# Kernel optimization log

Measured on AMD Instinct MI355X. Metric: run time of the kernel, lower is better.

The kernel has to match this reference:

```python
import jax, jax.numpy as jnp
import numpy as np

B, N, FEA = 4, 200000, 9
G = 32                      # per-axis index range used for voxel keys
NUM_SEG = B * G * G * G     # 131072 = max possible unique voxels (static)
OUT_DIM, COMPRE = 256, 16
BN_EPS = 1e-5

def _glorot(k, shape):
    lim = float(np.sqrt(6.0 / (shape[0] + shape[1])))
    return jax.random.uniform(k, shape, jnp.float32, -lim, lim)

def setup_inputs() -> dict:
    key = jax.random.key(0)
    ks = jax.random.split(key, 16)
    inp = {
        "pt_fea": jax.random.normal(ks[0], (B, N, FEA), jnp.float32),
        "xy_ind": jax.random.randint(ks[1], (B, N, 3), 0, G, dtype=jnp.int32),
    }
    dims = [FEA, 64, 128, 256, OUT_DIM]
    bn_dims = [FEA, 64, 128, 256]
    for i, d in enumerate(bn_dims):
        inp[f"bn{i}_g"] = jnp.ones((d,), jnp.float32)
        inp[f"bn{i}_b"] = jnp.zeros((d,), jnp.float32)
        inp[f"bn{i}_m"] = jax.random.normal(ks[2 + i], (d,), jnp.float32) * 0.1
        inp[f"bn{i}_v"] = jnp.ones((d,), jnp.float32)
    for i in range(4):
        inp[f"w{i+1}"] = _glorot(ks[6 + i], (dims[i], dims[i + 1]))
        inp[f"b{i+1}"] = jnp.zeros((dims[i + 1],), jnp.float32)
    inp["wc"] = _glorot(ks[10], (OUT_DIM, COMPRE))
    inp["bc"] = jnp.zeros((COMPRE,), jnp.float32)
    return inp

def _bn(x, g, b, m, v):
    return (x - m) * jax.lax.rsqrt(v + BN_EPS) * g + b

def reference(pt_fea, xy_ind, bn0_g, bn0_b, bn0_m, bn0_v,
              bn1_g, bn1_b, bn1_m, bn1_v, bn2_g, bn2_b, bn2_m, bn2_v,
              bn3_g, bn3_b, bn3_m, bn3_v,
              w1, b1, w2, b2, w3, b3, w4, b4, wc, bc):
    # flatten batched point clouds; build scalar voxel key = (batch, ix, iy, iz)
    b_idx = jnp.broadcast_to(jnp.arange(B, dtype=jnp.int32)[:, None], (B, N)).reshape(-1)
    ind = xy_ind.reshape(B * N, 3)
    keys = ((b_idx * G + ind[:, 0]) * G + ind[:, 1]) * G + ind[:, 2]  # [B*N]
    fea = pt_fea.reshape(B * N, FEA)

    # torch.unique(dim=0) equivalent: sorted unique keys + inverse map (static size)
    unq_keys, unq_inv = jnp.unique(keys, size=NUM_SEG, fill_value=-1, return_inverse=True)

    # torch_scatter.scatter_max over voxels
    pooled = jax.ops.segment_max(fea, unq_inv, num_segments=NUM_SEG)
    cnt = jax.ops.segment_sum(jnp.ones((B * N,), jnp.float32), unq_inv, num_segments=NUM_SEG)
    pooled = jnp.where(cnt[:, None] > 0, pooled, 0.0)  # neutralize empty padding slots (-inf)

    # PPmodel: BN -> Linear -> BN -> ReLU (x3) -> Linear (eval-mode BatchNorm)
    x = _bn(pooled, bn0_g, bn0_b, bn0_m, bn0_v)
    x = jax.nn.relu(_bn(x @ w1 + b1, bn1_g, bn1_b, bn1_m, bn1_v))
    x = jax.nn.relu(_bn(x @ w2 + b2, bn2_g, bn2_b, bn2_m, bn2_v))
    x = jax.nn.relu(_bn(x @ w3 + b3, bn3_g, bn3_b, bn3_m, bn3_v))
    x = x @ w4 + b4
    out = jax.nn.relu(x @ wc + bc)  # fea_compression

    # decode keys back to [num_vox, 4] int64 (batch, ix, iy, iz); padding rows = -1
    valid = unq_keys >= 0
    kk = jnp.where(valid, unq_keys, 0)
    unq = jnp.stack([kk // (G * G * G), (kk // (G * G)) % G, (kk // G) % G, kk % G], axis=1)
    unq = jnp.where(valid[:, None], unq, -1)
    return unq.astype(jnp.int64), out
```

## Files before the change

### kernel.cpp

```cpp
#include <hip/hip_runtime.h>

#define NPTS   800000
#define NPB    200000
#define NSEG   131072
#define OUT_OFF (NSEG*4)
#define BN_EPS 1e-5f
#define BCAP   3072

typedef __attribute__((ext_vector_type(8))) __bf16 bf16x8;
typedef __attribute__((ext_vector_type(4))) float  f32x4;

#define MFMA16 __builtin_amdgcn_mfma_f32_16x16x32_bf16

__device__ __forceinline__ unsigned short f2bf(float f) {
    unsigned u = __float_as_uint(f);
    u += 0x7fffu + ((u >> 16) & 1u);
    return (unsigned short)(u >> 16);
}
__device__ __forceinline__ unsigned encf(float f) {
    unsigned u = __float_as_uint(f);
    return (u & 0x80000000u) ? ~u : (u | 0x80000000u);
}
__device__ __forceinline__ float decf(unsigned e) {
    unsigned u = (e & 0x80000000u) ? (e & 0x7FFFFFFFu) : ~e;
    return __uint_as_float(u);
}

__global__ void k_fold(const float* __restrict__ g0, const float* __restrict__ be0,
                       const float* __restrict__ m0, const float* __restrict__ v0,
                       const float* __restrict__ g1, const float* __restrict__ be1,
                       const float* __restrict__ m1, const float* __restrict__ v1,
                       const float* __restrict__ g2, const float* __restrict__ be2,
                       const float* __restrict__ m2, const float* __restrict__ v2,
                       const float* __restrict__ g3, const float* __restrict__ be3,
                       const float* __restrict__ m3, const float* __restrict__ v3,
                       const float* __restrict__ w1, const float* __restrict__ b1,
                       const float* __restrict__ w2, const float* __restrict__ b2,
                       const float* __restrict__ w3, const float* __restrict__ b3,
                       const float* __restrict__ w4, const float* __restrict__ b4,
                       const float* __restrict__ wc, const float* __restrict__ bc,
                       unsigned short* __restrict__ WT1, float* __restrict__ c1,
                       unsigned short* __restrict__ WT2, float* __restrict__ c2,
                       unsigned short* __restrict__ WT3, float* __restrict__ c3,
                       unsigned short* __restrict__ WT4, float* __restrict__ c4,
                       unsigned* __restrict__ bucketFill) {
    int id = blockIdx.x * 256 + threadIdx.x;
    if (id < 32768) {
        int j = id >> 7, k = id & 127;
        float s = g3[j] * rsqrtf(v3[j] + BN_EPS);
        WT3[id] = f2bf(w3[k*256 + j] * s);
    } else if (id < 40960) {
        int t = id - 32768; int j = t >> 6, k = t & 63;
        float s = g2[j] * rsqrtf(v2[j] + BN_EPS);
        WT2[t] = f2bf(w2[k*128 + j] * s);
    } else if (id < 45056) {
        int t = id - 40960; int j = t >> 8, k = t & 255;
        float acc = 0.f;
        for (int i = 0; i < 256; ++i) acc += w4[k*256 + i] * wc[i*16 + j];
        WT4[t] = f2bf(acc);
    } else if (id < 47104) {
        int t = id - 45056; int j = t >> 5, k = t & 31;
        float val = 0.f;
        if (k < 9) {
            float s0 = g0[k] * rsqrtf(v0[k] + BN_EPS);
            float s1 = g1[j] * rsqrtf(v1[j] + BN_EPS);
            val = s0 * w1[k*64 + j] * s1;
        }
        WT1[t] = f2bf(val);
    } else if (id < 47168) {
        int j = id - 47104;
        float s1 = g1[j] * rsqrtf(v1[j] + BN_EPS);
        float acc = b1[j];
        for (int k = 0; k < 9; ++k) {
            float s0 = g0[k] * rsqrtf(v0[k] + BN_EPS);
            float t0 = be0[k] - m0[k] * s0;
            acc += t0 * w1[k*64 + j];
        }
        c1[j] = (acc - m1[j]) * s1 + be1[j];
    } else if (id < 47296) {
        int j = id - 47168;
        float s = g2[j] * rsqrtf(v2[j] + BN_EPS);
        c2[j] = (b2[j] - m2[j]) * s + be2[j];
    } else if (id < 47552) {
        int j = id - 47296;
        float s = g3[j] * rsqrtf(v3[j] + BN_EPS);
        c3[j] = (b3[j] - m3[j]) * s + be3[j];
    } else if (id < 47568) {
        int j = id - 47552;
        float acc = bc[j];
        for (int i = 0; i < 256; ++i) acc += b4[i] * wc[i*16 + j];
        c4[j] = acc;
    } else if (id < 48080) {
        bucketFill[id - 47568] = 0u;
    }
}

__global__ void kC(const int* __restrict__ ind, unsigned* __restrict__ bucketFill,
                   unsigned* __restrict__ bucketed) {
    __shared__ unsigned lh[512], gb[512];
    __shared__ unsigned stash[512*16];
    const int t = threadIdx.x;
    if (t < 512) lh[t] = 0u;
    __syncthreads();
    int bkt[4]; unsigned slot[4]; unsigned pay[4];
    #pragma unroll
    for (int i = 0; i < 4; ++i) {
        int p = blockIdx.x * 4096 + i * 1024 + t;
        if (p < NPTS) {
            int ix = ind[p*3], iy = ind[p*3+1], iz = ind[p*3+2];
            int b = p / NPB;
            bkt[i] = b*128 + ix*4 + (iy >> 3);
            pay[i] = ((unsigned)((iy & 7)*32 + iz) << 20) | (unsigned)p;
            slot[i] = atomicAdd(&lh[bkt[i]], 1u);
            if (slot[i] < 16u) stash[bkt[i]*16 + slot[i]] = pay[i];
        } else bkt[i] = -1;
    }
    __syncthreads();
    if (t < 512 && lh[t] > 0u) gb[t] = atomicAdd(&bucketFill[t], lh[t]);
    __syncthreads();
    for (int i = t; i < 512*16; i += 1024) {
        int b = i >> 4, e = i & 15;
        unsigned n = lh[b]; if (n > 16u) n = 16u;
        if ((unsigned)e < n) {
            unsigned pos = gb[b] + (unsigned)e;
            if (pos < BCAP) bucketed[b*BCAP + pos] = stash[i];
        }
    }
    #pragma unroll
    for (int i = 0; i < 4; ++i) if (bkt[i] >= 0 && slot[i] >= 16u) {
        unsigned pos = gb[bkt[i]] + slot[i];
        if (pos < BCAP) bucketed[bkt[i]*BCAP + pos] = pay[i];
    }
}

__global__ void kD(const float* __restrict__ fea,
                   const unsigned* __restrict__ bucketFill, const unsigned* __restrict__ bucketed,
                   float* __restrict__ pooledD, unsigned long long* __restrict__ occW) {
    __shared__ unsigned enc[256*9];
    const int t = threadIdx.x, bkt = blockIdx.x;
    for (int i = t; i < 2304; i += 1024) enc[i] = 0u;
    __syncthreads();
    unsigned n = bucketFill[bkt]; if (n > BCAP) n = BCAP;
    for (unsigned j = t; j < n; j += 1024) {
        unsigned e = bucketed[bkt*BCAP + j];
        unsigned p = e & 0xFFFFFu;
        unsigned v = e >> 20;
        const float* fp = fea + (size_t)p*9;
        #pragma unroll
        for (int f = 0; f < 9; ++f) atomicMax(&enc[v*9+f], encf(fp[f]));
    }
    __syncthreads();
    if (t < 256) {
        int occ = (enc[t*9] != 0u) ? 1 : 0;
        unsigned long long m = __ballot(occ);
        if ((t & 63) == 0) occW[bkt*4 + (t >> 6)] = m;
    }
    for (int e = t; e < 2304; e += 1024) {
        int v = e / 9;
        float val = (enc[v*9] != 0u) ? decf(enc[e]) : 0.f;
        pooledD[(size_t)(bkt*256 + v)*9 + (e - v*9)] = val;
    }
}

__global__ void kScan(const unsigned long long* __restrict__ occW,
                      unsigned* __restrict__ wordBase, unsigned* __restrict__ totSlot) {
    __shared__ unsigned s[512];
    const int t = threadIdx.x;
    unsigned c[4], sum = 0u;
    #pragma unroll
    for (int i = 0; i < 4; ++i) { c[i] = (unsigned)__popcll(occW[t*4+i]); sum += c[i]; }
    s[t] = sum;
    __syncthreads();
    for (int off = 1; off < 512; off <<= 1) {
        unsigned add = (t >= off) ? s[t-off] : 0u;
        __syncthreads();
        s[t] += add;
        __syncthreads();
    }
    unsigned run = s[t] - sum;
    #pragma unroll
    for (int i = 0; i < 4; ++i) { wordBase[t*4+i] = run; run += c[i]; }
    if (t == 511) totSlot[0] = s[511];
}


__device__ __forceinline__ void store4(char* base, int r, int strideElems, int n, f32x4 acc) {
    union { __bf16 h[4]; uint2 u; } pk;
    #pragma unroll
    for (int i = 0; i < 4; ++i) pk.h[i] = (__bf16)fmaxf(acc[i], 0.f);
    int s = n >> 3;
    *reinterpret_cast<uint2*>(base + r*strideElems*2 + ((s ^ (r & 7)) << 4) + (n & 4)*2) = pk.u;
}

__global__ void __launch_bounds__(512, 2)
k_mlp(const float* __restrict__ pooledD,
      const unsigned long long* __restrict__ occW,
      const unsigned* __restrict__ wordBase,
      const unsigned* __restrict__ totSlot,
      const unsigned short* __restrict__ WT1, const float* __restrict__ c1,
      const unsigned short* __restrict__ WT2, const float* __restrict__ c2,
      const unsigned short* __restrict__ WT3, const float* __restrict__ c3,
      const unsigned short* __restrict__ WT4, const float* __restrict__ c4,
      float* __restrict__ unqOut, float* __restrict__ outF) {
    __shared__ __align__(16) char lds[61440];
    char* Rin = lds;
    char* H1  = lds + 4096;
    char* H2  = lds + 12288;
    char* H3  = lds + 28672;
    const int tid = threadIdx.x;
    const int wv = tid >> 6, lane = tid & 63;
    const int r16 = lane & 15, kg = lane >> 4;

    for (int i = tid; i < 1024; i += 512) reinterpret_cast<unsigned*>(Rin)[i] = 0u;

    const int ft1 = wv & 3;
    bf16x8 a1 = *reinterpret_cast<const bf16x8*>(WT1 + (ft1*16 + r16)*32 + kg*8);
    f32x4 c1v = *reinterpret_cast<const f32x4*>(c1 + ft1*16 + kg*4);
    bf16x8 a2[2];
    #pragma unroll
    for (int ks = 0; ks < 2; ++ks)
        a2[ks] = *reinterpret_cast<const bf16x8*>(WT2 + (wv*16 + r16)*64 + ks*32 + kg*8);
    f32x4 c2v = *reinterpret_cast<const f32x4*>(c2 + wv*16 + kg*4);
    bf16x8 a3[2][4]; f32x4 c3v[2];
    #pragma unroll
    for (int u = 0; u < 2; ++u) {
        int ft = wv*2 + u;
        #pragma unroll
        for (int ks = 0; ks < 4; ++ks)
            a3[u][ks] = *reinterpret_cast<const bf16x8*>(WT3 + (ft*16 + r16)*128 + ks*32 + kg*8);
        c3v[u] = *reinterpret_cast<const f32x4*>(c3 + ft*16 + kg*4);
    }
    bf16x8 a4[8]; f32x4 c4v;
    if (wv < 4) {
        #pragma unroll
        for (int ks = 0; ks < 8; ++ks)
            a4[ks] = *reinterpret_cast<const bf16x8*>(WT4 + r16*256 + ks*32 + kg*8);
        c4v = *reinterpret_cast<const f32x4*>(c4 + kg*4);
    }
    const unsigned tot = totSlot[0];

    int tile = blockIdx.x;
    float pf0, pf1;
    {
        const float* src = pooledD + (size_t)tile * 576;
        pf0 = src[tid];
        pf1 = (tid < 64) ? src[512 + tid] : 0.f;
    }
    #pragma unroll 1
    for (int it = 0; it < 8; ++it) {
        {
            int r = tid / 9, c = tid - r*9;
            *reinterpret_cast<__bf16*>(Rin + r*64 + (((c>>3) ^ (r&3))<<4) + (c&7)*2) = (__bf16)pf0;
            if (tid < 64) {
                int j = 512 + tid; int r2 = j / 9, c2 = j - r2*9;
                *reinterpret_cast<__bf16*>(Rin + r2*64 + (((c2>>3) ^ (r2&3))<<4) + (c2&7)*2) = (__bf16)pf1;
            }
        }
        unsigned long long w = occW[tile];
        unsigned base = wordBase[tile];
        if (it < 7) {
            const float* src = pooledD + ((size_t)tile + 256) * 576;
            pf0 = src[tid];
            if (tid < 64) pf1 = src[512 + tid];
        }
        __syncthreads();
        {
            const int rtb = (wv >> 2) * 2;
            #pragma unroll
            for (int i = 0; i < 2; ++i) {
                int r = (rtb + i)*16 + r16;
                bf16x8 b = *reinterpret_cast<const bf16x8*>(Rin + r*64 + ((kg ^ (r&3))<<4));
                f32x4 acc = MFMA16(a1, b, c1v, 0, 0, 0);
                store4(H1, r, 64, ft1*16 + kg*4, acc);
            }
        }
        __syncthreads();
        #pragma unroll
        for (int rt = 0; rt < 4; ++rt) {
            int r = rt*16 + r16;
            bf16x8 b0 = *reinterpret_cast<const bf16x8*>(H1 + r*128 + ((kg ^ (r&7))<<4));
            bf16x8 b1 = *reinterpret_cast<const bf16x8*>(H1 + r*128 + (((4+kg) ^ (r&7))<<4));
            f32x4 acc = MFMA16(a2[0], b0, c2v, 0, 0, 0);
            acc = MFMA16(a2[1], b1, acc, 0, 0, 0);
            store4(H2, r, 128, wv*16 + kg*4, acc);
        }
        __syncthreads();
        #pragma unroll
        for (int rt = 0; rt < 4; ++rt) {
            int r = rt*16 + r16;
            bf16x8 b[4];
            #pragma unroll
            for (int ks = 0; ks < 4; ++ks)
                b[ks] = *reinterpret_cast<const bf16x8*>(H2 + r*256 + (((ks*4+kg) ^ (r&7))<<4));
            #pragma unroll
            for (int u = 0; u < 2; ++u) {
                f32x4 acc = c3v[u];
                #pragma unroll
                for (int ks = 0; ks < 4; ++ks)
                    acc = MFMA16(a3[u][ks], b[ks], acc, 0, 0, 0);
                store4(H3, r, 256, (wv*2+u)*16 + kg*4, acc);
            }
        }
        __syncthreads();
        if (wv < 4) {
            int r = wv*16 + r16;
            f32x4 acc = c4v;
            #pragma unroll
            for (int ks = 0; ks < 8; ++ks) {
                bf16x8 b = *reinterpret_cast<const bf16x8*>(H3 + r*512 + (((ks*4+kg) ^ (r&7))<<4));
                acc = MFMA16(a4[ks], b, acc, 0, 0, 0);
            }
            unsigned rdense = base + (unsigned)__popcll(w & ((1ull << r) - 1ull));
            unsigned rk = ((w >> r) & 1ull) ? rdense
                        : tot + (unsigned)(tile*64 + r) - rdense;
            float4 o;
            o.x = fmaxf(acc[0], 0.f); o.y = fmaxf(acc[1], 0.f);
            o.z = fmaxf(acc[2], 0.f); o.w = fmaxf(acc[3], 0.f);
            *reinterpret_cast<float4*>(outF + (size_t)rk*16 + kg*4) = o;
        } else if (wv == 4) {
            int r = lane, k = tile*64 + r;
            unsigned rdense = base + (unsigned)__popcll(w & ((1ull << r) - 1ull));
            if ((w >> r) & 1ull) {
                reinterpret_cast<float4*>(unqOut)[rdense] =
                    make_float4((float)(k >> 15), (float)((k >> 10) & 31),
                                (float)((k >> 5) & 31), (float)(k & 31));
            } else {
                unsigned er = tot + (unsigned)k - rdense;
                reinterpret_cast<float4*>(unqOut)[er] = make_float4(-1.f,-1.f,-1.f,-1.f);
            }
        }
        tile += 256;
    }
}

extern "C" void kernel_launch(void* const* d_in, const int* in_sizes, int n_in,
                              void* d_out, int out_size, void* d_ws, size_t ws_size,
                              hipStream_t stream) {
    const float* pt_fea = (const float*)d_in[0];
    const int*   xy_ind = (const int*)  d_in[1];
    const float* g0 = (const float*)d_in[2],  *be0 = (const float*)d_in[3];
    const float* m0 = (const float*)d_in[4],  *v0  = (const float*)d_in[5];
    const float* g1 = (const float*)d_in[6],  *be1 = (const float*)d_in[7];
    const float* m1 = (const float*)d_in[8],  *v1  = (const float*)d_in[9];
    const float* g2 = (const float*)d_in[10], *be2 = (const float*)d_in[11];
    const float* m2 = (const float*)d_in[12], *v2  = (const float*)d_in[13];
    const float* g3 = (const float*)d_in[14], *be3 = (const float*)d_in[15];
    const float* m3 = (const float*)d_in[16], *v3  = (const float*)d_in[17];
    const float* w1 = (const float*)d_in[18], *b1  = (const float*)d_in[19];
    const float* w2 = (const float*)d_in[20], *b2  = (const float*)d_in[21];
    const float* w3 = (const float*)d_in[22], *b3  = (const float*)d_in[23];
    const float* w4 = (const float*)d_in[24], *b4  = (const float*)d_in[25];
    const float* wc = (const float*)d_in[26], *bc  = (const float*)d_in[27];

    float* dout = (float*)d_out;

    unsigned* ws = (unsigned*)d_ws;
    unsigned long long* occW = (unsigned long long*)ws;
    unsigned* bucketFill = ws + 4096;
    unsigned* wordBase   = ws + 4608;
    unsigned* totSlot    = ws + 6656;
    unsigned* bucketed   = ws + 6664;
    float*    pooledD    = (float*)(bucketed + 512*BCAP);
    unsigned short* WT1  = (unsigned short*)(pooledD + (size_t)NSEG*9);
    unsigned short* WT2  = WT1 + 2048;
    unsigned short* WT3  = WT2 + 8192;
    unsigned short* WT4  = WT3 + 32768;
    float* c1 = (float*)(WT4 + 4096);
    float* c2 = c1 + 64;
    float* c3 = c2 + 128;
    float* c4 = c3 + 256;

    k_fold<<<188, 256, 0, stream>>>(g0,be0,m0,v0, g1,be1,m1,v1, g2,be2,m2,v2, g3,be3,m3,v3,
                                    w1,b1, w2,b2, w3,b3, w4,b4, wc,bc,
                                    WT1,c1, WT2,c2, WT3,c3, WT4,c4, bucketFill);
    kC<<<196, 1024, 0, stream>>>(xy_ind, bucketFill, bucketed);
    kD<<<512, 1024, 0, stream>>>(pt_fea, bucketFill, bucketed, pooledD, occW);
    kScan<<<1, 512, 0, stream>>>(occW, wordBase, totSlot);
    k_mlp<<<256, 512, 0, stream>>>(pooledD, occW, wordBase, totSlot,
                                   WT1,c1, WT2,c2, WT3,c3, WT4,c4, dout, dout + OUT_OFF);
}
```

Before: 68.12 us.

## Merge weight folding into bucketing kernel, fuse scan via last-block, widen MLP grid

Weight/BN folding now runs in extra blocks of the bucketing kernel, and bucket counters are zeroed with a memset. The separate scan kernel is replaced by a last-block-done pattern at the end of the pooling kernel, which uses an atomic ticket. The MLP kernel launches 512 blocks with higher occupancy bounds and loads its final-layer weights inside the loop to reduce register pressure. Together these cut two kernel launches and their serialization gaps, at the cost of an atomic/fence tail and repeated WT4 loads.

```diff
diff --git a/kernel.cpp b/kernel.cpp
--- a/kernel.cpp
+++ b/kernel.cpp
@@ -26,80 +26,81 @@
     return __uint_as_float(u);
 }
 
-__global__ void k_fold(const float* __restrict__ g0, const float* __restrict__ be0,
-                       const float* __restrict__ m0, const float* __restrict__ v0,
-                       const float* __restrict__ g1, const float* __restrict__ be1,
-                       const float* __restrict__ m1, const float* __restrict__ v1,
-                       const float* __restrict__ g2, const float* __restrict__ be2,
-                       const float* __restrict__ m2, const float* __restrict__ v2,
-                       const float* __restrict__ g3, const float* __restrict__ be3,
-                       const float* __restrict__ m3, const float* __restrict__ v3,
-                       const float* __restrict__ w1, const float* __restrict__ b1,
-                       const float* __restrict__ w2, const float* __restrict__ b2,
-                       const float* __restrict__ w3, const float* __restrict__ b3,
-                       const float* __restrict__ w4, const float* __restrict__ b4,
-                       const float* __restrict__ wc, const float* __restrict__ bc,
-                       unsigned short* __restrict__ WT1, float* __restrict__ c1,
-                       unsigned short* __restrict__ WT2, float* __restrict__ c2,
-                       unsigned short* __restrict__ WT3, float* __restrict__ c3,
-                       unsigned short* __restrict__ WT4, float* __restrict__ c4,
-                       unsigned* __restrict__ bucketFill) {
-    int id = blockIdx.x * 256 + threadIdx.x;
-    if (id < 32768) {
-        int j = id >> 7, k = id & 127;
-        float s = g3[j] * rsqrtf(v3[j] + BN_EPS);
-        WT3[id] = f2bf(w3[k*256 + j] * s);
-    } else if (id < 40960) {
-        int t = id - 32768; int j = t >> 6, k = t & 63;
-        float s = g2[j] * rsqrtf(v2[j] + BN_EPS);
-        WT2[t] = f2bf(w2[k*128 + j] * s);
-    } else if (id < 45056) {
-        int t = id - 40960; int j = t >> 8, k = t & 255;
-        float acc = 0.f;
-        for (int i = 0; i < 256; ++i) acc += w4[k*256 + i] * wc[i*16 + j];
-        WT4[t] = f2bf(acc);
-    } else if (id < 47104) {
-        int t = id - 45056; int j = t >> 5, k = t & 31;
-        float val = 0.f;
-        if (k < 9) {
-            float s0 = g0[k] * rsqrtf(v0[k] + BN_EPS);
-            float s1 = g1[j] * rsqrtf(v1[j] + BN_EPS);
-            val = s0 * w1[k*64 + j] * s1;
-        }
-        WT1[t] = f2bf(val);
-    } else if (id < 47168) {
-        int j = id - 47104;
-        float s1 = g1[j] * rsqrtf(v1[j] + BN_EPS);
-        float acc = b1[j];
-        for (int k = 0; k < 9; ++k) {
-            float s0 = g0[k] * rsqrtf(v0[k] + BN_EPS);
-            float t0 = be0[k] - m0[k] * s0;
-            acc += t0 * w1[k*64 + j];
-        }
-        c1[j] = (acc - m1[j]) * s1 + be1[j];
-    } else if (id < 47296) {
-        int j = id - 47168;
-        float s = g2[j] * rsqrtf(v2[j] + BN_EPS);
-        c2[j] = (b2[j] - m2[j]) * s + be2[j];
-    } else if (id < 47552) {
-        int j = id - 47296;
-        float s = g3[j] * rsqrtf(v3[j] + BN_EPS);
-        c3[j] = (b3[j] - m3[j]) * s + be3[j];
-    } else if (id < 47568) {
-        int j = id - 47552;
-        float acc = bc[j];
-        for (int i = 0; i < 256; ++i) acc += b4[i] * wc[i*16 + j];
-        c4[j] = acc;
-    } else if (id < 48080) {
-        bucketFill[id - 47568] = 0u;
-    }
-}
-
-__global__ void kC(const int* __restrict__ ind, unsigned* __restrict__ bucketFill,
-                   unsigned* __restrict__ bucketed) {
+__global__ void __launch_bounds__(1024)
+kA(const int* __restrict__ ind,
+   const float* __restrict__ g0, const float* __restrict__ be0,
+   const float* __restrict__ m0, const float* __restrict__ v0,
+   const float* __restrict__ g1, const float* __restrict__ be1,
+   const float* __restrict__ m1, const float* __restrict__ v1,
+   const float* __restrict__ g2, const float* __restrict__ be2,
+   const float* __restrict__ m2, const float* __restrict__ v2,
+   const float* __restrict__ g3, const float* __restrict__ be3,
+   const float* __restrict__ m3, const float* __restrict__ v3,
+   const float* __restrict__ w1, const float* __restrict__ b1,
+   const float* __restrict__ w2, const float* __restrict__ b2,
+   const float* __restrict__ w3, const float* __restrict__ b3,
+   const float* __restrict__ w4, const float* __restrict__ b4,
+   const float* __restrict__ wc, const float* __restrict__ bc,
+   unsigned short* __restrict__ WT1, float* __restrict__ c1,
+   unsigned short* __restrict__ WT2, float* __restrict__ c2,
+   unsigned short* __restrict__ WT3, float* __restrict__ c3,
+   unsigned short* __restrict__ WT4, float* __restrict__ c4,
+   unsigned* __restrict__ bucketFill, unsigned* __restrict__ bucketed) {
     __shared__ unsigned lh[512], gb[512];
     __shared__ unsigned stash[512*16];
     const int t = threadIdx.x;
+
+    if (blockIdx.x >= 196) {
+        int id = (blockIdx.x - 196) * 1024 + t;
+        if (id < 32768) {
+            int j = id >> 7, k = id & 127;
+            float s = g3[j] * rsqrtf(v3[j] + BN_EPS);
+            WT3[id] = f2bf(w3[k*256 + j] * s);
+        } else if (id < 40960) {
+            int q = id - 32768; int j = q >> 6, k = q & 63;
+            float s = g2[j] * rsqrtf(v2[j] + BN_EPS);
+            WT2[q] = f2bf(w2[k*128 + j] * s);
+        } else if (id < 45056) {
+            int q = id - 40960; int j = q >> 8, k = q & 255;
+            float acc = 0.f;
+            for (int i = 0; i < 256; ++i) acc += w4[k*256 + i] * wc[i*16 + j];
+            WT4[q] = f2bf(acc);
+        } else if (id < 47104) {
+            int q = id - 45056; int j = q >> 5, k = q & 31;
+            float val = 0.f;
+            if (k < 9) {
+                float s0 = g0[k] * rsqrtf(v0[k] + BN_EPS);
+                float s1 = g1[j] * rsqrtf(v1[j] + BN_EPS);
+                val = s0 * w1[k*64 + j] * s1;
+            }
+            WT1[q] = f2bf(val);
+        } else if (id < 47168) {
+            int j = id - 47104;
+            float s1 = g1[j] * rsqrtf(v1[j] + BN_EPS);
+            float acc = b1[j];
+            for (int k = 0; k < 9; ++k) {
+                float s0 = g0[k] * rsqrtf(v0[k] + BN_EPS);
+                float t0 = be0[k] - m0[k] * s0;
+                acc += t0 * w1[k*64 + j];
+            }
+            c1[j] = (acc - m1[j]) * s1 + be1[j];
+        } else if (id < 47296) {
+            int j = id - 47168;
+            float s = g2[j] * rsqrtf(v2[j] + BN_EPS);
+            c2[j] = (b2[j] - m2[j]) * s + be2[j];
+        } else if (id < 47552) {
+            int j = id - 47296;
+            float s = g3[j] * rsqrtf(v3[j] + BN_EPS);
+            c3[j] = (b3[j] - m3[j]) * s + be3[j];
+        } else if (id < 47568) {
+            int j = id - 47552;
+            float acc = bc[j];
+            for (int i = 0; i < 256; ++i) acc += b4[i] * wc[i*16 + j];
+            c4[j] = acc;
+        }
+        return;
+    }
+
     if (t < 512) lh[t] = 0u;
     __syncthreads();
     int bkt[4]; unsigned slot[4]; unsigned pay[4];
@@ -133,10 +134,15 @@
     }
 }
 
-__global__ void kD(const float* __restrict__ fea,
-                   const unsigned* __restrict__ bucketFill, const unsigned* __restrict__ bucketed,
-                   float* __restrict__ pooledD, unsigned long long* __restrict__ occW) {
+__global__ void __launch_bounds__(1024)
+kD(const float* __restrict__ fea,
+   const unsigned* __restrict__ bucketFill, const unsigned* __restrict__ bucketed,
+   float* __restrict__ pooledD, unsigned long long* __restrict__ occW,
+   unsigned* __restrict__ done, unsigned* __restrict__ wordBase,
+   unsigned* __restrict__ totSlot) {
     __shared__ unsigned enc[256*9];
+    __shared__ unsigned sScan[512];
+    __shared__ unsigned lastFlag;
     const int t = threadIdx.x, bkt = blockIdx.x;
     for (int i = t; i < 2304; i += 1024) enc[i] = 0u;
     __syncthreads();
@@ -160,27 +166,38 @@
         float val = (enc[v*9] != 0u) ? decf(enc[e]) : 0.f;
         pooledD[(size_t)(bkt*256 + v)*9 + (e - v*9)] = val;
     }
-}
-
-__global__ void kScan(const unsigned long long* __restrict__ occW,
-                      unsigned* __restrict__ wordBase, unsigned* __restrict__ totSlot) {
-    __shared__ unsigned s[512];
-    const int t = threadIdx.x;
+    __syncthreads();
+    if (t == 0) {
+        __threadfence();
+        unsigned tk = __hip_atomic_fetch_add(done, 1u, __ATOMIC_ACQ_REL, __HIP_MEMORY_SCOPE_AGENT);
+        lastFlag = (tk == 511u) ? 1u : 0u;
+    }
+    __syncthreads();
+    if (!lastFlag) return;
     unsigned c[4], sum = 0u;
-    #pragma unroll
-    for (int i = 0; i < 4; ++i) { c[i] = (unsigned)__popcll(occW[t*4+i]); sum += c[i]; }
-    s[t] = sum;
+    if (t < 512) {
+        #pragma unroll
+        for (int i = 0; i < 4; ++i) {
+            unsigned long long w =
+                __hip_atomic_load(&occW[t*4+i], __ATOMIC_ACQUIRE, __HIP_MEMORY_SCOPE_AGENT);
+            c[i] = (unsigned)__popcll(w);
+            sum += c[i];
+        }
+        sScan[t] = sum;
+    }
     __syncthreads();
     for (int off = 1; off < 512; off <<= 1) {
-        unsigned add = (t >= off) ? s[t-off] : 0u;
-        __syncthreads();
-        s[t] += add;
-        __syncthreads();
-    }
-    unsigned run = s[t] - sum;
-    #pragma unroll
-    for (int i = 0; i < 4; ++i) { wordBase[t*4+i] = run; run += c[i]; }
-    if (t == 511) totSlot[0] = s[511];
+        unsigned add = (t >= off && t < 512) ? sScan[t-off] : 0u;
+        __syncthreads();
+        if (t < 512) sScan[t] += add;
+        __syncthreads();
+    }
+    if (t < 512) {
+        unsigned run = sScan[t] - sum;
+        #pragma unroll
+        for (int i = 0; i < 4; ++i) { wordBase[t*4+i] = run; run += c[i]; }
+        if (t == 511) totSlot[0] = run;
+    }
 }
 
 
@@ -192,7 +209,7 @@
     *reinterpret_cast<uint2*>(base + r*strideElems*2 + ((s ^ (r & 7)) << 4) + (n & 4)*2) = pk.u;
 }
 
-__global__ void __launch_bounds__(512, 2)
+__global__ void __launch_bounds__(512, 4)
 k_mlp(const float* __restrict__ pooledD,
       const unsigned long long* __restrict__ occW,
       const unsigned* __restrict__ wordBase,
@@ -230,14 +247,8 @@
             a3[u][ks] = *reinterpret_cast<const bf16x8*>(WT3 + (ft*16 + r16)*128 + ks*32 + kg*8);
         c3v[u] = *reinterpret_cast<const f32x4*>(c3 + ft*16 + kg*4);
     }
-    bf16x8 a4[8]; f32x4 c4v;
-    if (wv < 4) {
-        #pragma unroll
-        for (int ks = 0; ks < 8; ++ks)
-            a4[ks] = *reinterpret_cast<const bf16x8*>(WT4 + r16*256 + ks*32 + kg*8);
-        c4v = *reinterpret_cast<const f32x4*>(c4 + kg*4);
-    }
     const unsigned tot = totSlot[0];
+    __syncthreads();
 
     int tile = blockIdx.x;
     float pf0, pf1;
@@ -247,7 +258,7 @@
         pf1 = (tid < 64) ? src[512 + tid] : 0.f;
     }
     #pragma unroll 1
-    for (int it = 0; it < 8; ++it) {
+    for (int it = 0; it < 4; ++it) {
         {
             int r = tid / 9, c = tid - r*9;
             *reinterpret_cast<__bf16*>(Rin + r*64 + (((c>>3) ^ (r&3))<<4) + (c&7)*2) = (__bf16)pf0;
@@ -258,8 +269,8 @@
         }
         unsigned long long w = occW[tile];
         unsigned base = wordBase[tile];
-        if (it < 7) {
-            const float* src = pooledD + ((size_t)tile + 256) * 576;
+        if (it < 3) {
+            const float* src = pooledD + ((size_t)tile + 512) * 576;
             pf0 = src[tid];
             if (tid < 64) pf1 = src[512 + tid];
         }
@@ -288,18 +299,22 @@
         #pragma unroll
         for (int rt = 0; rt < 4; ++rt) {
             int r = rt*16 + r16;
-            bf16x8 b[4];
+            f32x4 acc0 = c3v[0], acc1 = c3v[1];
             #pragma unroll
-            for (int ks = 0; ks < 4; ++ks)
-                b[ks] = *reinterpret_cast<const bf16x8*>(H2 + r*256 + (((ks*4+kg) ^ (r&7))<<4));
+            for (int ks = 0; ks < 4; ++ks) {
+                bf16x8 b = *reinterpret_cast<const bf16x8*>(H2 + r*256 + (((ks*4+kg) ^ (r&7))<<4));
+                acc0 = MFMA16(a3[0][ks], b, acc0, 0, 0, 0);
+                acc1 = MFMA16(a3[1][ks], b, acc1, 0, 0, 0);
+            }
+            store4(H3, r, 256, (wv*2+0)*16 + kg*4, acc0);
+            store4(H3, r, 256, (wv*2+1)*16 + kg*4, acc1);
+        }
+        bf16x8 a4[8]; f32x4 c4v;
+        if (wv < 4) {
             #pragma unroll
-            for (int u = 0; u < 2; ++u) {
-                f32x4 acc = c3v[u];
-                #pragma unroll
-                for (int ks = 0; ks < 4; ++ks)
-                    acc = MFMA16(a3[u][ks], b[ks], acc, 0, 0, 0);
-                store4(H3, r, 256, (wv*2+u)*16 + kg*4, acc);
-            }
+            for (int ks = 0; ks < 8; ++ks)
+                a4[ks] = *reinterpret_cast<const bf16x8*>(WT4 + r16*256 + ks*32 + kg*8);
+            c4v = *reinterpret_cast<const f32x4*>(c4 + kg*4);
         }
         __syncthreads();
         if (wv < 4) {
@@ -329,7 +344,7 @@
                 reinterpret_cast<float4*>(unqOut)[er] = make_float4(-1.f,-1.f,-1.f,-1.f);
             }
         }
-        tile += 256;
+        tile += 512;
     }
 }
 
@@ -354,12 +369,13 @@
 
     float* dout = (float*)d_out;
 
-    unsigned* ws = (unsigned*)d_ws;
-    unsigned long long* occW = (unsigned long long*)ws;
-    unsigned* bucketFill = ws + 4096;
-    unsigned* wordBase   = ws + 4608;
-    unsigned* totSlot    = ws + 6656;
-    unsigned* bucketed   = ws + 6664;
+    unsigned* ws0 = (unsigned*)d_ws;
+    unsigned long long* occW = (unsigned long long*)ws0;
+    unsigned* bucketFill = ws0 + 4096;
+    unsigned* done       = ws0 + 4608;
+    unsigned* wordBase   = ws0 + 4616;
+    unsigned* totSlot    = ws0 + 6664;
+    unsigned* bucketed   = ws0 + 6672;
     float*    pooledD    = (float*)(bucketed + 512*BCAP);
     unsigned short* WT1  = (unsigned short*)(pooledD + (size_t)NSEG*9);
     unsigned short* WT2  = WT1 + 2048;
@@ -370,12 +386,14 @@
     float* c3 = c2 + 128;
     float* c4 = c3 + 256;
 
-    k_fold<<<188, 256, 0, stream>>>(g0,be0,m0,v0, g1,be1,m1,v1, g2,be2,m2,v2, g3,be3,m3,v3,
-                                    w1,b1, w2,b2, w3,b3, w4,b4, wc,bc,
-                                    WT1,c1, WT2,c2, WT3,c3, WT4,c4, bucketFill);
-    kC<<<196, 1024, 0, stream>>>(xy_ind, bucketFill, bucketed);
-    kD<<<512, 1024, 0, stream>>>(pt_fea, bucketFill, bucketed, pooledD, occW);
-    kScan<<<1, 512, 0, stream>>>(occW, wordBase, totSlot);
-    k_mlp<<<256, 512, 0, stream>>>(pooledD, occW, wordBase, totSlot,
+    hipMemsetAsync(bucketFill, 0, (512 + 8) * sizeof(unsigned), stream);
+    kA<<<243, 1024, 0, stream>>>(xy_ind,
+                                 g0,be0,m0,v0, g1,be1,m1,v1, g2,be2,m2,v2, g3,be3,m3,v3,
+                                 w1,b1, w2,b2, w3,b3, w4,b4, wc,bc,
+                                 WT1,c1, WT2,c2, WT3,c3, WT4,c4,
+                                 bucketFill, bucketed);
+    kD<<<512, 1024, 0, stream>>>(pt_fea, bucketFill, bucketed, pooledD, occW,
+                                 done, wordBase, totSlot);
+    k_mlp<<<512, 512, 0, stream>>>(pooledD, occW, wordBase, totSlot,
                                    WT1,c1, WT2,c2, WT3,c3, WT4,c4, dout, dout + OUT_OFF);
 }
```

Result: slower. 151.1 us (+121.8%).

## Shrink kC blocks to local bucket windows and vectorize kD feature loads

Applied to the files above, without the earlier changes.

kC now gives each 512-thread block 2048 consecutive points. Such a block touches at most two batches, so it keeps a 256-bucket local histogram and stash with 32 entries per bucket instead of 512 buckets with 16 entries. This launches more, smaller blocks, uses less LDS per block and cuts the scattered global writes that overflow the stash. kD reads each point's 9 features with two float4 loads plus one scalar load instead of nine scalar loads; those float4 loads are often not 16-byte aligned. A __syncthreads was also added in k_mlp and the bucketed buffer offset was shifted to a 16-word boundary.

```diff
diff --git a/kernel.cpp b/kernel.cpp
--- a/kernel.cpp
+++ b/kernel.cpp
@@ -6,6 +6,8 @@
 #define OUT_OFF (NSEG*4)
 #define BN_EPS 1e-5f
 #define BCAP   3072
+#define KC_PTS 2048
+#define KC_CAP 32
 
 typedef __attribute__((ext_vector_type(8))) __bf16 bf16x8;
 typedef __attribute__((ext_vector_type(4))) float  f32x4;
@@ -95,47 +97,51 @@
     }
 }
 
-__global__ void kC(const int* __restrict__ ind, unsigned* __restrict__ bucketFill,
-                   unsigned* __restrict__ bucketed) {
-    __shared__ unsigned lh[512], gb[512];
-    __shared__ unsigned stash[512*16];
+__global__ void __launch_bounds__(512)
+kC(const int* __restrict__ ind, unsigned* __restrict__ bucketFill,
+   unsigned* __restrict__ bucketed) {
+    __shared__ unsigned lh[256], gb[256];
+    __shared__ unsigned stash[256*KC_CAP];
     const int t = threadIdx.x;
-    if (t < 512) lh[t] = 0u;
-    __syncthreads();
-    int bkt[4]; unsigned slot[4]; unsigned pay[4];
+    const int base = blockIdx.x * KC_PTS;
+    const int b0 = base / NPB;
+    if (t < 256) lh[t] = 0u;
+    __syncthreads();
+    int loc[4]; unsigned slot[4]; unsigned pay[4];
     #pragma unroll
     for (int i = 0; i < 4; ++i) {
-        int p = blockIdx.x * 4096 + i * 1024 + t;
+        int p = base + i*512 + t;
         if (p < NPTS) {
             int ix = ind[p*3], iy = ind[p*3+1], iz = ind[p*3+2];
             int b = p / NPB;
-            bkt[i] = b*128 + ix*4 + (iy >> 3);
+            loc[i] = (b - b0)*128 + ix*4 + (iy >> 3);
             pay[i] = ((unsigned)((iy & 7)*32 + iz) << 20) | (unsigned)p;
-            slot[i] = atomicAdd(&lh[bkt[i]], 1u);
-            if (slot[i] < 16u) stash[bkt[i]*16 + slot[i]] = pay[i];
-        } else bkt[i] = -1;
-    }
-    __syncthreads();
-    if (t < 512 && lh[t] > 0u) gb[t] = atomicAdd(&bucketFill[t], lh[t]);
-    __syncthreads();
-    for (int i = t; i < 512*16; i += 1024) {
-        int b = i >> 4, e = i & 15;
-        unsigned n = lh[b]; if (n > 16u) n = 16u;
+            slot[i] = atomicAdd(&lh[loc[i]], 1u);
+            if (slot[i] < KC_CAP) stash[loc[i]*KC_CAP + slot[i]] = pay[i];
+        } else loc[i] = -1;
+    }
+    __syncthreads();
+    if (t < 256 && lh[t] > 0u) gb[t] = atomicAdd(&bucketFill[b0*128 + t], lh[t]);
+    __syncthreads();
+    for (int i = t; i < 256*KC_CAP; i += 512) {
+        int s = i >> 5, e = i & (KC_CAP-1);
+        unsigned n = lh[s]; if (n > KC_CAP) n = KC_CAP;
         if ((unsigned)e < n) {
-            unsigned pos = gb[b] + (unsigned)e;
-            if (pos < BCAP) bucketed[b*BCAP + pos] = stash[i];
-        }
-    }
-    #pragma unroll
-    for (int i = 0; i < 4; ++i) if (bkt[i] >= 0 && slot[i] >= 16u) {
-        unsigned pos = gb[bkt[i]] + slot[i];
-        if (pos < BCAP) bucketed[bkt[i]*BCAP + pos] = pay[i];
-    }
-}
-
-__global__ void kD(const float* __restrict__ fea,
-                   const unsigned* __restrict__ bucketFill, const unsigned* __restrict__ bucketed,
-                   float* __restrict__ pooledD, unsigned long long* __restrict__ occW) {
+            unsigned pos = gb[s] + (unsigned)e;
+            if (pos < BCAP) bucketed[(size_t)(b0*128 + s)*BCAP + pos] = stash[i];
+        }
+    }
+    #pragma unroll
+    for (int i = 0; i < 4; ++i) if (loc[i] >= 0 && slot[i] >= KC_CAP) {
+        unsigned pos = gb[loc[i]] + slot[i];
+        if (pos < BCAP) bucketed[(size_t)(b0*128 + loc[i])*BCAP + pos] = pay[i];
+    }
+}
+
+__global__ void __launch_bounds__(1024)
+kD(const float* __restrict__ fea,
+   const unsigned* __restrict__ bucketFill, const unsigned* __restrict__ bucketed,
+   float* __restrict__ pooledD, unsigned long long* __restrict__ occW) {
     __shared__ unsigned enc[256*9];
     const int t = threadIdx.x, bkt = blockIdx.x;
     for (int i = t; i < 2304; i += 1024) enc[i] = 0u;
@@ -146,8 +152,15 @@
         unsigned p = e & 0xFFFFFu;
         unsigned v = e >> 20;
         const float* fp = fea + (size_t)p*9;
-        #pragma unroll
-        for (int f = 0; f < 9; ++f) atomicMax(&enc[v*9+f], encf(fp[f]));
+        float4 q0 = *reinterpret_cast<const float4*>(fp);
+        float4 q1 = *reinterpret_cast<const float4*>(fp + 4);
+        float  f8 = fp[8];
+        unsigned* eb = enc + v*9;
+        atomicMax(eb+0, encf(q0.x)); atomicMax(eb+1, encf(q0.y));
+        atomicMax(eb+2, encf(q0.z)); atomicMax(eb+3, encf(q0.w));
+        atomicMax(eb+4, encf(q1.x)); atomicMax(eb+5, encf(q1.y));
+        atomicMax(eb+6, encf(q1.z)); atomicMax(eb+7, encf(q1.w));
+        atomicMax(eb+8, encf(f8));
     }
     __syncthreads();
     if (t < 256) {
@@ -238,6 +251,7 @@
         c4v = *reinterpret_cast<const f32x4*>(c4 + kg*4);
     }
     const unsigned tot = totSlot[0];
+    __syncthreads();
 
     int tile = blockIdx.x;
     float pf0, pf1;
@@ -354,12 +368,12 @@
 
     float* dout = (float*)d_out;
 
-    unsigned* ws = (unsigned*)d_ws;
-    unsigned long long* occW = (unsigned long long*)ws;
-    unsigned* bucketFill = ws + 4096;
-    unsigned* wordBase   = ws + 4608;
-    unsigned* totSlot    = ws + 6656;
-    unsigned* bucketed   = ws + 6664;
+    unsigned* ws0 = (unsigned*)d_ws;
+    unsigned long long* occW = (unsigned long long*)ws0;
+    unsigned* bucketFill = ws0 + 4096;
+    unsigned* wordBase   = ws0 + 4608;
+    unsigned* totSlot    = ws0 + 6656;
+    unsigned* bucketed   = ws0 + 6672;
     float*    pooledD    = (float*)(bucketed + 512*BCAP);
     unsigned short* WT1  = (unsigned short*)(pooledD + (size_t)NSEG*9);
     unsigned short* WT2  = WT1 + 2048;
@@ -373,7 +387,7 @@
     k_fold<<<188, 256, 0, stream>>>(g0,be0,m0,v0, g1,be1,m1,v1, g2,be2,m2,v2, g3,be3,m3,v3,
                                     w1,b1, w2,b2, w3,b3, w4,b4, wc,bc,
                                     WT1,c1, WT2,c2, WT3,c3, WT4,c4, bucketFill);
-    kC<<<196, 1024, 0, stream>>>(xy_ind, bucketFill, bucketed);
+    kC<<<(NPTS + KC_PTS - 1)/KC_PTS, 512, 0, stream>>>(xy_ind, bucketFill, bucketed);
     kD<<<512, 1024, 0, stream>>>(pt_fea, bucketFill, bucketed, pooledD, occW);
     kScan<<<1, 512, 0, stream>>>(occW, wordBase, totSlot);
     k_mlp<<<256, 512, 0, stream>>>(pooledD, occW, wordBase, totSlot,
```

Result: no change. 69.08 us (+1.4%).
